# Kernel tuning notes

Measured on AMD Instinct MI355X. Metric: run time of the kernel, lower is better.

The kernel has to match this reference:

```python
import jax, jax.numpy as jnp
import numpy as np

N = 50000      # nodes
E = 800000     # edges
D = 200        # in_dim = hid_dim
R = 230        # num_rels
B = 100        # bdd bases -> submat = D // B = 2
S = D // B     # submatrix size (2)


def setup_inputs() -> dict:
    key = jax.random.key(0)
    ks = jax.random.split(key, 16)
    node_feat = jax.random.normal(ks[0], (N, D), dtype=jnp.float32)
    dynamic_emb = jax.random.normal(ks[1], (N, 1, D), dtype=jnp.float32)
    src = jax.random.randint(ks[2], (E,), 0, N, dtype=jnp.int32)
    dst = jax.random.randint(ks[3], (E,), 0, N, dtype=jnp.int32)
    etypes = jax.random.randint(ks[4], (E,), 0, R, dtype=jnp.int32)
    # BDD relational weights per layer: [R, B, S, S]
    w1 = jax.random.normal(ks[5], (R, B, S, S), dtype=jnp.float32) * 0.1
    loop_w1 = jax.random.normal(ks[6], (D, D), dtype=jnp.float32) * 0.05
    b1 = jnp.zeros((D,), dtype=jnp.float32)
    w2 = jax.random.normal(ks[7], (R, B, S, S), dtype=jnp.float32) * 0.1
    loop_w2 = jax.random.normal(ks[8], (D, D), dtype=jnp.float32) * 0.05
    b2 = jnp.zeros((D,), dtype=jnp.float32)
    # single-layer vanilla RNN (tanh) params
    W_ih = jax.random.normal(ks[9], (D, D), dtype=jnp.float32) * 0.05
    W_hh = jax.random.normal(ks[10], (D, D), dtype=jnp.float32) * 0.05
    b_ih = jnp.zeros((D,), dtype=jnp.float32)
    b_hh = jnp.zeros((D,), dtype=jnp.float32)
    return {"node_feat": node_feat, "dynamic_emb": dynamic_emb,
            "src": src, "dst": dst, "etypes": etypes,
            "w1": w1, "loop_w1": loop_w1, "b1": b1,
            "w2": w2, "loop_w2": loop_w2, "b2": b2,
            "W_ih": W_ih, "W_hh": W_hh, "b_ih": b_ih, "b_hh": b_hh}


def _rel_graph_conv_bdd(x, src, dst, etypes, edge_norm, w, loop_w, b):
    # gather source feats and apply per-edge-type block-diagonal transform
    xs = x[src].reshape(E, B, S)                     # [E, B, S]
    msg = jnp.einsum('ebi,ebio->ebo', xs, w[etypes]) # [E, B, S]
    msg = msg.reshape(E, D) * edge_norm              # edge-norm scaling
    agg = jax.ops.segment_sum(msg, dst, num_segments=N)  # scatter-add to dst
    return agg + x @ loop_w + b                      # self-loop + bias


def reference(node_feat, dynamic_emb, src, dst, etypes,
              w1, loop_w1, b1, w2, loop_w2, b2,
              W_ih, W_hh, b_ih, b_hh):
    # edge_norm = dst node norm = 1 / in-degree
    deg = jax.ops.segment_sum(jnp.ones((E,), jnp.float32), dst, num_segments=N)
    node_norm = jnp.where(deg > 0, 1.0 / jnp.maximum(deg, 1.0), 0.0)
    edge_norm = node_norm[dst][:, None]              # [E, 1]

    # RGCN layer 1 (tanh activation), layer 2 (no activation); dropout=eval
    h = _rel_graph_conv_bdd(node_feat, src, dst, etypes, edge_norm, w1, loop_w1, b1)
    h = jnp.tanh(h)
    h = _rel_graph_conv_bdd(h, src, dst, etypes, edge_norm, w2, loop_w2, b2)

    # single-step vanilla RNN: hn = tanh(x W_ih^T + b_ih + h0 W_hh^T + b_hh)
    h0 = dynamic_emb[:, 0, :]                        # [N, D]
    hn = jnp.tanh(h @ W_ih.T + b_ih + h0 @ W_hh.T + b_hh)
    return hn[:, None, :]                            # [N, 1, D]
```

## Files before the change

### kernel.cpp

```cpp
#include <hip/hip_runtime.h>

#define N_NODES 50000
#define N_EDGES 800000
#define DIM     200
#define NBLK    100
#define NRELS   230
#define NB_SCAN 196
#define KPAD    224
#define KPN     256
#define NROWPAD 50048
#define NFRAG8  (8 * 14 * 64)

typedef __attribute__((ext_vector_type(8)))  short short8;
typedef __attribute__((ext_vector_type(16))) float f32x16;

__device__ __forceinline__ unsigned short f2bf(float f) {
    unsigned u = __float_as_uint(f);
    u += 0x7fffu + ((u >> 16) & 1u);
    return (unsigned short)(u >> 16);
}

__device__ __forceinline__ float bflo(unsigned u) { return __uint_as_float(u << 16); }
__device__ __forceinline__ float bfhi(unsigned u) { return __uint_as_float(u & 0xffff0000u); }
__device__ __forceinline__ float b2f(unsigned short u) { return __uint_as_float((unsigned)u << 16); }

__device__ __forceinline__ float tanh_fast(float x) {
    float xa = fminf(fmaxf(x, -15.0f), 15.0f);
    float e = __expf(2.0f * xa);
    return (e - 1.0f) / (e + 1.0f);
}

__device__ __forceinline__ int uread(int v, int l) {
    return __builtin_amdgcn_readlane(v, l);
}

#if __has_builtin(__builtin_amdgcn_fdot2_f32_bf16)
typedef __bf16 bf16x2 __attribute__((ext_vector_type(2)));
__device__ __forceinline__ float dot2bf(unsigned a, unsigned b, float c) {
    return __builtin_amdgcn_fdot2_f32_bf16(
        __builtin_bit_cast(bf16x2, a), __builtin_bit_cast(bf16x2, b), c, false);
}
#define CMP(XU, WU, M0, M1, M2, M3)                                     \
    { M0 = dot2bf(XU.x, WU.x, M0); M1 = dot2bf(XU.x, WU.y, M1);         \
      M2 = dot2bf(XU.y, WU.z, M2); M3 = dot2bf(XU.y, WU.w, M3); }
#else
#define CMP(XU, WU, M0, M1, M2, M3)                                     \
    { float x0 = bflo(XU.x), x1 = bfhi(XU.x);                           \
      float x2 = bflo(XU.y), x3 = bfhi(XU.y);                           \
      M0 += x0 * bflo(WU.x) + x1 * bfhi(WU.x);                          \
      M1 += x0 * bflo(WU.y) + x1 * bfhi(WU.y);                          \
      M2 += x2 * bflo(WU.z) + x3 * bfhi(WU.z);                          \
      M3 += x2 * bflo(WU.w) + x3 * bfhi(WU.w); }
#endif

#define SWZ5(rr, off) ((unsigned)((rr) * 512 + (off)) ^ ((unsigned)((rr) & 15) << 4))

__global__ void deg_int_kernel(const int* __restrict__ dst, int* __restrict__ degi) {
    int e = blockIdx.x * blockDim.x + threadIdx.x;
    if (e < N_EDGES) atomicAdd(&degi[dst[e]], 1);
}

__global__ __launch_bounds__(256) void scanA(const int* __restrict__ degi,
                                             int* __restrict__ pos,
                                             int* __restrict__ bsum) {
    __shared__ int tmp[256];
    int t = threadIdx.x;
    int g = blockIdx.x * 256 + t;
    int v = (g < N_NODES) ? degi[g] : 0;
    tmp[t] = v;
    __syncthreads();
    for (int off = 1; off < 256; off <<= 1) {
        int xv = (t >= off) ? tmp[t - off] : 0;
        __syncthreads();
        tmp[t] += xv;
        __syncthreads();
    }
    if (g < N_NODES) pos[g] = tmp[t] - v;
    if (t == 255) bsum[blockIdx.x] = tmp[255];
}

__global__ __launch_bounds__(256) void scanB(int* __restrict__ bsum) {
    __shared__ int tmp[256];
    int t = threadIdx.x;
    int v = (t < NB_SCAN) ? bsum[t] : 0;
    tmp[t] = v;
    __syncthreads();
    for (int off = 1; off < 256; off <<= 1) {
        int xv = (t >= off) ? tmp[t - off] : 0;
        __syncthreads();
        tmp[t] += xv;
        __syncthreads();
    }
    if (t < NB_SCAN) bsum[t] = tmp[t] - v;
}

__global__ __launch_bounds__(256) void scanC(int* __restrict__ pos, const int* __restrict__ bsum) {
    int g = blockIdx.x * 256 + threadIdx.x;
    if (g < N_NODES) pos[g] += bsum[blockIdx.x];
}

__global__ void fill_kernel(const int* __restrict__ src, const int* __restrict__ dst,
                            const int* __restrict__ et,
                            int* __restrict__ pos, int* __restrict__ se) {
    int e = blockIdx.x * blockDim.x + threadIdx.x;
    if (e < N_EDGES) {
        int d = dst[e];
        int slot = atomicAdd(&pos[d], 1);
        se[slot] = src[e] | (et[e] << 16);
    }
}

__global__ void prep_xb(const float* __restrict__ x, unsigned short* __restrict__ o) {
    int idx = blockIdx.x * blockDim.x + threadIdx.x;
    if (idx >= NROWPAD * (KPAD / 2)) return;
    int row = idx / (KPAD / 2), cu = idx % (KPAD / 2);
    unsigned pk = 0;
    if (row < N_NODES && cu < 100) {
        float2 v = *(const float2*)(x + (size_t)row * DIM + cu * 2);
        pk = (unsigned)f2bf(v.x) | ((unsigned)f2bf(v.y) << 16);
    }
    *(unsigned*)(o + (size_t)idx * 2) = pk;
}

__global__ void prep_wb(const float* __restrict__ w, unsigned short* __restrict__ o) {
    int idx = blockIdx.x * blockDim.x + threadIdx.x;
    if (idx >= NRELS * NBLK) return;
    float4 v = *(const float4*)(w + (size_t)idx * 4);
    unsigned c0 = (unsigned)f2bf(v.x) | ((unsigned)f2bf(v.z) << 16);
    unsigned c1 = (unsigned)f2bf(v.y) | ((unsigned)f2bf(v.w) << 16);
    *(uint2*)(o + (size_t)idx * 4) = make_uint2(c0, c1);
}

__global__ void prep_fragT(const float* __restrict__ w, unsigned short* __restrict__ o) {
    int idx = blockIdx.x * blockDim.x + threadIdx.x;
    if (idx >= NFRAG8) return;
    int l = idx & 63;
    int ks = (idx >> 6) % 14;
    int nt = idx / (14 * 64);
    int n  = nt * 32 + (l & 31);
    int k0 = ks * 16 + (l >> 5) * 8;
    unsigned short v[8];
    #pragma unroll
    for (int j = 0; j < 8; ++j) {
        int k = k0 + j;
        v[j] = f2bf((n < DIM && k < DIM) ? w[k * DIM + n] : 0.0f);
    }
    *(uint4*)(o + (size_t)idx * 8) = *(uint4*)v;
}
__global__ void prep_frag(const float* __restrict__ w, unsigned short* __restrict__ o) {
    int idx = blockIdx.x * blockDim.x + threadIdx.x;
    if (idx >= NFRAG8) return;
    int l = idx & 63;
    int ks = (idx >> 6) % 14;
    int nt = idx / (14 * 64);
    int n  = nt * 32 + (l & 31);
    int k0 = ks * 16 + (l >> 5) * 8;
    unsigned short v[8];
    #pragma unroll
    for (int j = 0; j < 8; ++j) {
        int k = k0 + j;
        v[j] = f2bf((n < DIM && k < DIM) ? w[n * DIM + k] : 0.0f);
    }
    *(uint4*)(o + (size_t)idx * 8) = *(uint4*)v;
}

#define GL(QQ, XU, WU)                                                  \
    { int p_ = uread(sv, (QQ)); int s_ = p_ & 0xffff; int r_ = p_ >> 16;\
      XU = *(const uint2*)(x  + (size_t)s_ * KPAD + xoff);              \
      WU = *(const uint4*)(wb + (size_t)r_ * (NBLK * 4) + woff); }

__global__ __launch_bounds__(256) void gatherB(
        const unsigned short* __restrict__ x,
        const int*   __restrict__ se,
        const int*   __restrict__ endpos,
        const int*   __restrict__ degi,
        const unsigned short* __restrict__ wb,
        unsigned short* __restrict__ agg) {
    int node = (blockIdx.x * blockDim.x + threadIdx.x) >> 6;
    int lane = threadIdx.x & 63;
    if (node >= N_NODES) return;
    int deg = __builtin_amdgcn_readfirstlane(degi[node]);
    const bool act = (lane < 50);
    int cl   = act ? lane : 49;
    int xoff = 4 * cl;
    int woff = 8 * cl;

    if (deg == 0) {
        if (act) *(uint2*)(agg + (size_t)node * DIM + 4 * lane) = make_uint2(0u, 0u);
        return;
    }
    int end   = __builtin_amdgcn_readfirstlane(endpos[node]);
    int start = end - deg;

    float m0A = 0.f, m1A = 0.f, m2A = 0.f, m3A = 0.f;
    float m0B = 0.f, m1B = 0.f, m2B = 0.f, m3B = 0.f;

    for (int base = start; base < end; base += 64) {
        int cnt = end - base; if (cnt > 64) cnt = 64;
        int sv = se[base + (lane < cnt ? lane : cnt - 1)];

        uint2 X0 = {0,0}, X1 = {0,0}, X2 = {0,0}, X3 = {0,0};
        uint4 W0 = {0,0,0,0}, W1 = {0,0,0,0}, W2 = {0,0,0,0}, W3 = {0,0,0,0};

        GL(0, X0, W0);
        if (cnt > 1) GL(1, X1, W1);
        if (cnt > 2) GL(2, X2, W2);

        for (int q = 0; q < cnt; q += 4) {
            if (q + 3 < cnt) GL(q + 3, X3, W3);
            CMP(X0, W0, m0A, m1A, m2A, m3A);
            if (q + 4 < cnt) GL(q + 4, X0, W0);
            if (q + 1 < cnt) CMP(X1, W1, m0B, m1B, m2B, m3B);
            if (q + 5 < cnt) GL(q + 5, X1, W1);
            if (q + 2 < cnt) CMP(X2, W2, m0A, m1A, m2A, m3A);
            if (q + 6 < cnt) GL(q + 6, X2, W2);
            if (q + 3 < cnt) CMP(X3, W3, m0B, m1B, m2B, m3B);
        }
    }
    float nrm = 1.0f / (float)deg;
    if (act) {
        unsigned plo = (unsigned)f2bf((m0A + m0B) * nrm) | ((unsigned)f2bf((m1A + m1B) * nrm) << 16);
        unsigned phi = (unsigned)f2bf((m2A + m2B) * nrm) | ((unsigned)f2bf((m3A + m3B) * nrm) << 16);
        *(uint2*)(agg + (size_t)node * DIM + 4 * lane) = make_uint2(plo, phi);
    }
}

__global__ __launch_bounds__(256) void gemm1_kernel(
        unsigned short* xb_hb,
        const unsigned short* __restrict__ agg1,
        const float* __restrict__ b1,
        const unsigned short* __restrict__ w1f) {
    __shared__ __align__(16) unsigned short s_a[32 * KPN];
    int row0 = blockIdx.x * 32;
    int tid = threadIdx.x;
    for (int i = tid; i < 32 * 32; i += 256) {
        int rr = i >> 5, ch = i & 31;
        uint4 v = {0, 0, 0, 0};
        if (ch < 28) v = *(const uint4*)(xb_hb + (size_t)(row0 + rr) * KPAD + ch * 8);
        *(uint4*)((char*)s_a + SWZ5(rr, ch * 16)) = v;
    }
    __syncthreads();

    int l = tid & 63, wv = tid >> 6;
    int rl = l & 31, hl = l >> 5;
    int ntlo = wv * 2;
    const unsigned short* wb = w1f + (size_t)(ntlo * 14) * 512 + l * 8;

    f32x16 acc0 = {}, acc1 = {};
    short8 aC  = *(const short8*)((const char*)s_a + SWZ5(rl, (hl * 8) * 2));
    short8 b0C = *(const short8*)(wb);
    short8 b1C = *(const short8*)(wb + 14 * 512);
    #pragma unroll
    for (int ks = 0; ks < 13; ++ks) {
        short8 aN = {}, b0N = {}, b1N = {};
        if (ks < 12) {
            aN  = *(const short8*)((const char*)s_a + SWZ5(rl, ((ks + 1) * 16 + hl * 8) * 2));
            b0N = *(const short8*)(wb + (ks + 1) * 512);
            b1N = *(const short8*)(wb + 14 * 512 + (ks + 1) * 512);
        }
        acc0 = __builtin_amdgcn_mfma_f32_32x32x16_bf16(aC, b0C, acc0, 0, 0, 0);
        acc1 = __builtin_amdgcn_mfma_f32_32x32x16_bf16(aC, b1C, acc1, 0, 0, 0);
        aC = aN; b0C = b0N; b1C = b1N;
    }
    __syncthreads();

    #pragma unroll
    for (int t = 0; t < 2; ++t) {
        f32x16 ac = t ? acc1 : acc0;
        int gc = (ntlo + t) * 32 + rl;
        if (gc >= KPAD) continue;
        float bias = (gc < DIM) ? b1[gc] : 0.0f;
        #pragma unroll
        for (int r = 0; r < 16; ++r) {
            int gr = row0 + (r & 3) + 8 * (r >> 2) + 4 * hl;
            float v = 0.0f;
            if (gc < DIM && gr < N_NODES)
                v = ac[r] + b2f(agg1[(size_t)gr * DIM + gc]) + bias;
            xb_hb[(size_t)gr * KPAD + gc] = f2bf(tanh_fast(v));
        }
    }
}

__global__ __launch_bounds__(256) void gemm2_kernel(
        const unsigned short* __restrict__ hb,
        const unsigned short* __restrict__ agg2,
        const float* __restrict__ b2,
        const unsigned short* __restrict__ w2f,
        const unsigned short* __restrict__ h0b,
        const unsigned short* __restrict__ wihf,
        const unsigned short* __restrict__ whhf,
        const float* __restrict__ b_ih,
        const float* __restrict__ b_hh,
        float* __restrict__ out) {
    __shared__ __align__(16) unsigned short s_a[32 * KPN];
    __shared__ __align__(16) unsigned short t_lds[32 * KPN];
    int row0 = blockIdx.x * 32;
    int tid = threadIdx.x;
    int l = tid & 63, wv = tid >> 6;
    int rl = l & 31, hl = l >> 5;
    int ntlo = wv * 2;

    for (int i = tid; i < 32 * 32; i += 256) {
        int rr = i >> 5, ch = i & 31;
        uint4 v = {0, 0, 0, 0};
        if (ch < 28) v = *(const uint4*)(hb + (size_t)(row0 + rr) * KPAD + ch * 8);
        *(uint4*)((char*)s_a + SWZ5(rr, ch * 16)) = v;
    }
    __syncthreads();

    {
        const unsigned short* wb = w2f + (size_t)(ntlo * 14) * 512 + l * 8;
        f32x16 acc0 = {}, acc1 = {};
        short8 aC  = *(const short8*)((const char*)s_a + SWZ5(rl, (hl * 8) * 2));
        short8 b0C = *(const short8*)(wb);
        short8 b1C = *(const short8*)(wb + 14 * 512);
        #pragma unroll
        for (int ks = 0; ks < 13; ++ks) {
            short8 aN = {}, b0N = {}, b1N = {};
            if (ks < 12) {
                aN  = *(const short8*)((const char*)s_a + SWZ5(rl, ((ks + 1) * 16 + hl * 8) * 2));
                b0N = *(const short8*)(wb + (ks + 1) * 512);
                b1N = *(const short8*)(wb + 14 * 512 + (ks + 1) * 512);
            }
            acc0 = __builtin_amdgcn_mfma_f32_32x32x16_bf16(aC, b0C, acc0, 0, 0, 0);
            acc1 = __builtin_amdgcn_mfma_f32_32x32x16_bf16(aC, b1C, acc1, 0, 0, 0);
            aC = aN; b0C = b0N; b1C = b1N;
        }
        #pragma unroll
        for (int t = 0; t < 2; ++t) {
            f32x16 ac = t ? acc1 : acc0;
            int gc = (ntlo + t) * 32 + rl;
            float bias = (gc < DIM) ? b2[gc] : 0.0f;
            #pragma unroll
            for (int r = 0; r < 16; ++r) {
                int lr = (r & 3) + 8 * (r >> 2) + 4 * hl;
                int gr = row0 + lr;
                float v = 0.0f;
                if (gc < DIM) {
                    v = ac[r] + bias;
                    if (gr < N_NODES) v += b2f(agg2[(size_t)gr * DIM + gc]);
                }
                *(unsigned short*)((char*)t_lds + SWZ5(lr, gc * 2)) = f2bf(v);
            }
        }
    }
    __syncthreads();

    for (int i = tid; i < 32 * 32; i += 256) {
        int rr = i >> 5, ch = i & 31;
        uint4 v = {0, 0, 0, 0};
        if (ch < 28) v = *(const uint4*)(h0b + (size_t)(row0 + rr) * KPAD + ch * 8);
        *(uint4*)((char*)s_a + SWZ5(rr, ch * 16)) = v;
    }
    __syncthreads();

    {
        const unsigned short* wi = wihf + (size_t)(ntlo * 14) * 512 + l * 8;
        const unsigned short* wh = whhf + (size_t)(ntlo * 14) * 512 + l * 8;
        f32x16 o0 = {}, o1 = {};
        short8 tC  = *(const short8*)((const char*)t_lds + SWZ5(rl, (hl * 8) * 2));
        short8 fC  = *(const short8*)((const char*)s_a  + SWZ5(rl, (hl * 8) * 2));
        short8 i0C = *(const short8*)(wi);
        short8 i1C = *(const short8*)(wi + 14 * 512);
        short8 h0C = *(const short8*)(wh);
        short8 h1C = *(const short8*)(wh + 14 * 512);
        #pragma unroll
        for (int ks = 0; ks < 13; ++ks) {
            short8 tN = {}, fN = {}, i0N = {}, i1N = {}, h0N = {}, h1N = {};
            if (ks < 12) {
                unsigned off = ((ks + 1) * 16 + hl * 8) * 2;
                tN  = *(const short8*)((const char*)t_lds + SWZ5(rl, off));
                fN  = *(const short8*)((const char*)s_a  + SWZ5(rl, off));
                i0N = *(const short8*)(wi + (ks + 1) * 512);
                i1N = *(const short8*)(wi + 14 * 512 + (ks + 1) * 512);
                h0N = *(const short8*)(wh + (ks + 1) * 512);
                h1N = *(const short8*)(wh + 14 * 512 + (ks + 1) * 512);
            }
            o0 = __builtin_amdgcn_mfma_f32_32x32x16_bf16(tC, i0C, o0, 0, 0, 0);
            o0 = __builtin_amdgcn_mfma_f32_32x32x16_bf16(fC, h0C, o0, 0, 0, 0);
            o1 = __builtin_amdgcn_mfma_f32_32x32x16_bf16(tC, i1C, o1, 0, 0, 0);
            o1 = __builtin_amdgcn_mfma_f32_32x32x16_bf16(fC, h1C, o1, 0, 0, 0);
            tC = tN; fC = fN; i0C = i0N; i1C = i1N; h0C = h0N; h1C = h1N;
        }
        #pragma unroll
        for (int t = 0; t < 2; ++t) {
            f32x16 oc = t ? o1 : o0;
            int gc = (ntlo + t) * 32 + rl;
            if (gc >= DIM) continue;
            float bias = b_ih[gc] + b_hh[gc];
            #pragma unroll
            for (int r = 0; r < 16; ++r) {
                int gr = row0 + (r & 3) + 8 * (r >> 2) + 4 * hl;
                if (gr < N_NODES)
                    out[(size_t)gr * DIM + gc] = tanh_fast(oc[r] + bias);
            }
        }
    }
}

extern "C" void kernel_launch(void* const* d_in, const int* in_sizes, int n_in,
                              void* d_out, int out_size, void* d_ws, size_t ws_size,
                              hipStream_t stream) {
    const float* node_feat = (const float*)d_in[0];
    const float* dyn_emb   = (const float*)d_in[1];
    const int*   src       = (const int*)  d_in[2];
    const int*   dst       = (const int*)  d_in[3];
    const int*   etypes    = (const int*)  d_in[4];
    const float* w1        = (const float*)d_in[5];
    const float* loop_w1   = (const float*)d_in[6];
    const float* b1        = (const float*)d_in[7];
    const float* w2        = (const float*)d_in[8];
    const float* loop_w2   = (const float*)d_in[9];
    const float* b2        = (const float*)d_in[10];
    const float* W_ih      = (const float*)d_in[11];
    const float* W_hh      = (const float*)d_in[12];
    const float* b_ih      = (const float*)d_in[13];
    const float* b_hh      = (const float*)d_in[14];
    float* out = (float*)d_out;

    int*   degi = (int*)d_ws;
    int*   pos  = degi + 51200;
    int*   bsum = pos  + 51200;
    int*   se   = bsum + 256;
    unsigned short* agg = (unsigned short*)(se + N_EDGES);
    unsigned short* hb   = agg  + (size_t)N_NODES * DIM;
    unsigned short* h0b  = hb   + (size_t)NROWPAD * KPAD;
    unsigned short* w1f  = h0b  + (size_t)NROWPAD * KPAD;
    unsigned short* w2f  = w1f  + (size_t)NFRAG8 * 8;
    unsigned short* wihf = w2f  + (size_t)NFRAG8 * 8;
    unsigned short* whhf = wihf + (size_t)NFRAG8 * 8;
    unsigned short* w1b  = whhf + (size_t)NFRAG8 * 8;
    unsigned short* w2b  = w1b  + (size_t)NRELS * NBLK * 4;

    hipMemsetAsync(degi, 0, 51200 * sizeof(int), stream);

    deg_int_kernel<<<(N_EDGES + 255) / 256, 256, 0, stream>>>(dst, degi);
    scanA<<<NB_SCAN, 256, 0, stream>>>(degi, pos, bsum);
    scanB<<<1, 256, 0, stream>>>(bsum);
    scanC<<<NB_SCAN, 256, 0, stream>>>(pos, bsum);
    fill_kernel<<<(N_EDGES + 255) / 256, 256, 0, stream>>>(src, dst, etypes, pos, se);

    prep_xb<<<(NROWPAD * (KPAD / 2) + 255) / 256, 256, 0, stream>>>(node_feat, hb);
    prep_xb<<<(NROWPAD * (KPAD / 2) + 255) / 256, 256, 0, stream>>>(dyn_emb, h0b);
    prep_wb<<<(NRELS * NBLK + 255) / 256, 256, 0, stream>>>(w1, w1b);
    prep_wb<<<(NRELS * NBLK + 255) / 256, 256, 0, stream>>>(w2, w2b);
    prep_fragT<<<(NFRAG8 + 255) / 256, 256, 0, stream>>>(loop_w1, w1f);
    prep_fragT<<<(NFRAG8 + 255) / 256, 256, 0, stream>>>(loop_w2, w2f);
    prep_frag <<<(NFRAG8 + 255) / 256, 256, 0, stream>>>(W_ih, wihf);
    prep_frag <<<(NFRAG8 + 255) / 256, 256, 0, stream>>>(W_hh, whhf);

    gatherB<<<(N_NODES * 64 + 255) / 256, 256, 0, stream>>>(
        hb, se, pos, degi, w1b, agg);
    gemm1_kernel<<<(N_NODES + 31) / 32, 256, 0, stream>>>(
        hb, agg, b1, w1f);

    gatherB<<<(N_NODES * 64 + 255) / 256, 256, 0, stream>>>(
        hb, se, pos, degi, w2b, agg);

    gemm2_kernel<<<(N_NODES + 31) / 32, 256, 0, stream>>>(
        hb, agg, b2, w2f, h0b, wihf, whhf, b_ih, b_hh, out);
}
```

Before: 348.2 us.

## Fold layer-2 self-loop weight into RNN input weight and merge prep kernels

Precomputes M = loop_w2 · W_ih^T and a combined bias so the final kernel computes h·M + agg·W_ih^T + h0·W_hh^T in one MFMA pass. This removes the intermediate bf16 tile in LDS, one sync phase and a separate GEMM stage. The agg buffer becomes KPAD-padded so it can be staged like the other operands. Several small prep and scan launches are also merged into fewer kernels. In exchange, the final kernel issues three MFMAs per k-step instead of two sequential GEMMs, and the folded weights are rounded differently (M is rounded to bf16 once rather than the intermediate result).

Measured after the change: 367.8 us. 1.06x slower.

```diff
diff --git a/kernel.cpp b/kernel.cpp
--- a/kernel.cpp
+++ b/kernel.cpp
@@ -79,8 +79,9 @@
     if (t == 255) bsum[blockIdx.x] = tmp[255];
 }
 
-__global__ __launch_bounds__(256) void scanB(int* __restrict__ bsum) {
+__global__ __launch_bounds__(256) void scanC2(int* __restrict__ pos, const int* __restrict__ bsum) {
     __shared__ int tmp[256];
+    __shared__ int excl[256];
     int t = threadIdx.x;
     int v = (t < NB_SCAN) ? bsum[t] : 0;
     tmp[t] = v;
@@ -91,12 +92,11 @@
         tmp[t] += xv;
         __syncthreads();
     }
-    if (t < NB_SCAN) bsum[t] = tmp[t] - v;
-}
-
-__global__ __launch_bounds__(256) void scanC(int* __restrict__ pos, const int* __restrict__ bsum) {
-    int g = blockIdx.x * 256 + threadIdx.x;
-    if (g < N_NODES) pos[g] += bsum[blockIdx.x];
+    excl[t] = tmp[t] - v;
+    __syncthreads();
+    int add = excl[blockIdx.x];
+    int g = blockIdx.x * 256 + t;
+    if (g < N_NODES) pos[g] += add;
 }
 
 __global__ void fill_kernel(const int* __restrict__ src, const int* __restrict__ dst,
@@ -110,58 +110,97 @@
     }
 }
 
-__global__ void prep_xb(const float* __restrict__ x, unsigned short* __restrict__ o) {
+__global__ void prep_feat(const float* __restrict__ x, const float* __restrict__ de,
+                          unsigned short* __restrict__ hb, unsigned short* __restrict__ h0b) {
+    const int HALF = NROWPAD * (KPAD / 2);
     int idx = blockIdx.x * blockDim.x + threadIdx.x;
-    if (idx >= NROWPAD * (KPAD / 2)) return;
-    int row = idx / (KPAD / 2), cu = idx % (KPAD / 2);
+    if (idx >= 2 * HALF) return;
+    const float* src = (idx < HALF) ? x : de;
+    unsigned short* dstp = (idx < HALF) ? hb : h0b;
+    int j = (idx < HALF) ? idx : idx - HALF;
+    int row = j / (KPAD / 2), cu = j % (KPAD / 2);
     unsigned pk = 0;
     if (row < N_NODES && cu < 100) {
-        float2 v = *(const float2*)(x + (size_t)row * DIM + cu * 2);
+        float2 v = *(const float2*)(src + (size_t)row * DIM + cu * 2);
         pk = (unsigned)f2bf(v.x) | ((unsigned)f2bf(v.y) << 16);
     }
-    *(unsigned*)(o + (size_t)idx * 2) = pk;
-}
-
-__global__ void prep_wb(const float* __restrict__ w, unsigned short* __restrict__ o) {
+    *(unsigned*)(dstp + (size_t)j * 2) = pk;
+}
+
+__global__ void prep_wbs(const float* __restrict__ w1, const float* __restrict__ w2,
+                         unsigned short* __restrict__ w1b, unsigned short* __restrict__ w2b) {
+    const int HALF = NRELS * NBLK;
     int idx = blockIdx.x * blockDim.x + threadIdx.x;
-    if (idx >= NRELS * NBLK) return;
-    float4 v = *(const float4*)(w + (size_t)idx * 4);
+    if (idx >= 2 * HALF) return;
+    const float* w = (idx < HALF) ? w1 : w2;
+    unsigned short* o = (idx < HALF) ? w1b : w2b;
+    int j = (idx < HALF) ? idx : idx - HALF;
+    float4 v = *(const float4*)(w + (size_t)j * 4);
     unsigned c0 = (unsigned)f2bf(v.x) | ((unsigned)f2bf(v.z) << 16);
     unsigned c1 = (unsigned)f2bf(v.y) | ((unsigned)f2bf(v.w) << 16);
-    *(uint2*)(o + (size_t)idx * 4) = make_uint2(c0, c1);
-}
-
-__global__ void prep_fragT(const float* __restrict__ w, unsigned short* __restrict__ o) {
+    *(uint2*)(o + (size_t)j * 4) = make_uint2(c0, c1);
+}
+
+__global__ void prep_frags(const float* __restrict__ lw1, const float* __restrict__ wih,
+                           const float* __restrict__ whh,
+                           unsigned short* __restrict__ w1f, unsigned short* __restrict__ wihf,
+                           unsigned short* __restrict__ whhf) {
     int idx = blockIdx.x * blockDim.x + threadIdx.x;
-    if (idx >= NFRAG8) return;
-    int l = idx & 63;
-    int ks = (idx >> 6) % 14;
-    int nt = idx / (14 * 64);
+    if (idx >= 3 * NFRAG8) return;
+    int sec = idx / NFRAG8, f = idx % NFRAG8;
+    const float* w = (sec == 0) ? lw1 : (sec == 1) ? wih : whh;
+    unsigned short* o = (sec == 0) ? w1f : (sec == 1) ? wihf : whhf;
+    int l = f & 63;
+    int ks = (f >> 6) % 14;
+    int nt = f / (14 * 64);
     int n  = nt * 32 + (l & 31);
     int k0 = ks * 16 + (l >> 5) * 8;
     unsigned short v[8];
     #pragma unroll
     for (int j = 0; j < 8; ++j) {
         int k = k0 + j;
-        v[j] = f2bf((n < DIM && k < DIM) ? w[k * DIM + n] : 0.0f);
-    }
-    *(uint4*)(o + (size_t)idx * 8) = *(uint4*)v;
-}
-__global__ void prep_frag(const float* __restrict__ w, unsigned short* __restrict__ o) {
+        float val = 0.0f;
+        if (n < DIM && k < DIM)
+            val = (sec == 0) ? w[k * DIM + n] : w[n * DIM + k];
+        v[j] = f2bf(val);
+    }
+    *(uint4*)(o + (size_t)f * 8) = *(uint4*)v;
+}
+
+__global__ void prep_Mf(const float* __restrict__ w2, const float* __restrict__ wih,
+                        const float* __restrict__ b2, const float* __restrict__ b_ih,
+                        const float* __restrict__ b_hh,
+                        unsigned short* __restrict__ Mf, float* __restrict__ biasv) {
     int idx = blockIdx.x * blockDim.x + threadIdx.x;
-    if (idx >= NFRAG8) return;
-    int l = idx & 63;
-    int ks = (idx >> 6) % 14;
-    int nt = idx / (14 * 64);
-    int n  = nt * 32 + (l & 31);
-    int k0 = ks * 16 + (l >> 5) * 8;
-    unsigned short v[8];
-    #pragma unroll
-    for (int j = 0; j < 8; ++j) {
-        int k = k0 + j;
-        v[j] = f2bf((n < DIM && k < DIM) ? w[n * DIM + k] : 0.0f);
-    }
-    *(uint4*)(o + (size_t)idx * 8) = *(uint4*)v;
+    if (idx < NFRAG8) {
+        int l = idx & 63;
+        int ks = (idx >> 6) % 14;
+        int nt = idx / (14 * 64);
+        int n  = nt * 32 + (l & 31);
+        int k0 = ks * 16 + (l >> 5) * 8;
+        unsigned short v[8];
+        #pragma unroll
+        for (int j = 0; j < 8; ++j) {
+            int k = k0 + j;
+            float s = 0.0f;
+            if (n < DIM && k < DIM) {
+                const float* wr = w2 + (size_t)k * DIM;
+                const float* ir = wih + (size_t)n * DIM;
+                for (int q = 0; q < DIM; ++q) s += wr[q] * ir[q];
+            }
+            v[j] = f2bf(s);
+        }
+        *(uint4*)(Mf + (size_t)idx * 8) = *(uint4*)v;
+    } else if (idx < NFRAG8 + KPN) {
+        int n = idx - NFRAG8;
+        float s = 0.0f;
+        if (n < DIM) {
+            const float* ir = wih + (size_t)n * DIM;
+            for (int q = 0; q < DIM; ++q) s += b2[q] * ir[q];
+            s += b_ih[n] + b_hh[n];
+        }
+        biasv[n] = s;
+    }
 }
 
 #define GL(QQ, XU, WU)                                                  \
@@ -186,7 +225,7 @@
     int woff = 8 * cl;
 
     if (deg == 0) {
-        if (act) *(uint2*)(agg + (size_t)node * DIM + 4 * lane) = make_uint2(0u, 0u);
+        if (lane < 56) *(uint2*)(agg + (size_t)node * KPAD + 4 * lane) = make_uint2(0u, 0u);
         return;
     }
     int end   = __builtin_amdgcn_readfirstlane(endpos[node]);
@@ -218,11 +257,12 @@
         }
     }
     float nrm = 1.0f / (float)deg;
+    uint2 ov = make_uint2(0u, 0u);
     if (act) {
-        unsigned plo = (unsigned)f2bf((m0A + m0B) * nrm) | ((unsigned)f2bf((m1A + m1B) * nrm) << 16);
-        unsigned phi = (unsigned)f2bf((m2A + m2B) * nrm) | ((unsigned)f2bf((m3A + m3B) * nrm) << 16);
-        *(uint2*)(agg + (size_t)node * DIM + 4 * lane) = make_uint2(plo, phi);
-    }
+        ov.x = (unsigned)f2bf((m0A + m0B) * nrm) | ((unsigned)f2bf((m1A + m1B) * nrm) << 16);
+        ov.y = (unsigned)f2bf((m2A + m2B) * nrm) | ((unsigned)f2bf((m3A + m3B) * nrm) << 16);
+    }
+    if (lane < 56) *(uint2*)(agg + (size_t)node * KPAD + 4 * lane) = ov;
 }
 
 __global__ __launch_bounds__(256) void gemm1_kernel(
@@ -275,7 +315,7 @@
             int gr = row0 + (r & 3) + 8 * (r >> 2) + 4 * hl;
             float v = 0.0f;
             if (gc < DIM && gr < N_NODES)
-                v = ac[r] + b2f(agg1[(size_t)gr * DIM + gc]) + bias;
+                v = ac[r] + b2f(agg1[(size_t)gr * KPAD + gc]) + bias;
             xb_hb[(size_t)gr * KPAD + gc] = f2bf(tanh_fast(v));
         }
     }
@@ -283,117 +323,89 @@
 
 __global__ __launch_bounds__(256) void gemm2_kernel(
         const unsigned short* __restrict__ hb,
-        const unsigned short* __restrict__ agg2,
-        const float* __restrict__ b2,
-        const unsigned short* __restrict__ w2f,
+        const unsigned short* __restrict__ aggp,
         const unsigned short* __restrict__ h0b,
+        const unsigned short* __restrict__ Mf,
         const unsigned short* __restrict__ wihf,
         const unsigned short* __restrict__ whhf,
-        const float* __restrict__ b_ih,
-        const float* __restrict__ b_hh,
+        const float* __restrict__ biasv,
         float* __restrict__ out) {
-    __shared__ __align__(16) unsigned short s_a[32 * KPN];
-    __shared__ __align__(16) unsigned short t_lds[32 * KPN];
+    __shared__ __align__(16) unsigned short s_h[32 * KPN];
+    __shared__ __align__(16) unsigned short s_g[32 * KPN];
+    __shared__ __align__(16) unsigned short s_e[32 * KPN];
     int row0 = blockIdx.x * 32;
     int tid = threadIdx.x;
+    for (int i = tid; i < 32 * 32; i += 256) {
+        int rr = i >> 5, ch = i & 31;
+        uint4 vh = {0,0,0,0}, vg = {0,0,0,0}, ve = {0,0,0,0};
+        if (ch < 28) {
+            size_t off = (size_t)(row0 + rr) * KPAD + ch * 8;
+            vh = *(const uint4*)(hb   + off);
+            vg = *(const uint4*)(aggp + off);
+            ve = *(const uint4*)(h0b  + off);
+        }
+        unsigned sw = SWZ5(rr, ch * 16);
+        *(uint4*)((char*)s_h + sw) = vh;
+        *(uint4*)((char*)s_g + sw) = vg;
+        *(uint4*)((char*)s_e + sw) = ve;
+    }
+    __syncthreads();
+
     int l = tid & 63, wv = tid >> 6;
     int rl = l & 31, hl = l >> 5;
     int ntlo = wv * 2;
-
-    for (int i = tid; i < 32 * 32; i += 256) {
-        int rr = i >> 5, ch = i & 31;
-        uint4 v = {0, 0, 0, 0};
-        if (ch < 28) v = *(const uint4*)(hb + (size_t)(row0 + rr) * KPAD + ch * 8);
-        *(uint4*)((char*)s_a + SWZ5(rr, ch * 16)) = v;
-    }
-    __syncthreads();
-
-    {
-        const unsigned short* wb = w2f + (size_t)(ntlo * 14) * 512 + l * 8;
-        f32x16 acc0 = {}, acc1 = {};
-        short8 aC  = *(const short8*)((const char*)s_a + SWZ5(rl, (hl * 8) * 2));
-        short8 b0C = *(const short8*)(wb);
-        short8 b1C = *(const short8*)(wb + 14 * 512);
+    const unsigned short* pm = Mf   + (size_t)(ntlo * 14) * 512 + l * 8;
+    const unsigned short* pi = wihf + (size_t)(ntlo * 14) * 512 + l * 8;
+    const unsigned short* ph = whhf + (size_t)(ntlo * 14) * 512 + l * 8;
+
+    f32x16 a0 = {}, a1 = {};
+    unsigned off0 = SWZ5(rl, (hl * 8) * 2);
+    short8 hC  = *(const short8*)((const char*)s_h + off0);
+    short8 gC  = *(const short8*)((const char*)s_g + off0);
+    short8 eC  = *(const short8*)((const char*)s_e + off0);
+    short8 m0C = *(const short8*)(pm);
+    short8 m1C = *(const short8*)(pm + 14 * 512);
+    short8 i0C = *(const short8*)(pi);
+    short8 i1C = *(const short8*)(pi + 14 * 512);
+    short8 h0C = *(const short8*)(ph);
+    short8 h1C = *(const short8*)(ph + 14 * 512);
+    #pragma unroll
+    for (int ks = 0; ks < 13; ++ks) {
+        short8 hN = {}, gN = {}, eN = {};
+        short8 m0N = {}, m1N = {}, i0N = {}, i1N = {}, h0N = {}, h1N = {};
+        if (ks < 12) {
+            unsigned off = SWZ5(rl, ((ks + 1) * 16 + hl * 8) * 2);
+            hN  = *(const short8*)((const char*)s_h + off);
+            gN  = *(const short8*)((const char*)s_g + off);
+            eN  = *(const short8*)((const char*)s_e + off);
+            m0N = *(const short8*)(pm + (ks + 1) * 512);
+            m1N = *(const short8*)(pm + 14 * 512 + (ks + 1) * 512);
+            i0N = *(const short8*)(pi + (ks + 1) * 512);
+            i1N = *(const short8*)(pi + 14 * 512 + (ks + 1) * 512);
+            h0N = *(const short8*)(ph + (ks + 1) * 512);
+            h1N = *(const short8*)(ph + 14 * 512 + (ks + 1) * 512);
+        }
+        a0 = __builtin_amdgcn_mfma_f32_32x32x16_bf16(hC, m0C, a0, 0, 0, 0);
+        a0 = __builtin_amdgcn_mfma_f32_32x32x16_bf16(gC, i0C, a0, 0, 0, 0);
+        a0 = __builtin_amdgcn_mfma_f32_32x32x16_bf16(eC, h0C, a0, 0, 0, 0);
+        a1 = __builtin_amdgcn_mfma_f32_32x32x16_bf16(hC, m1C, a1, 0, 0, 0);
+        a1 = __builtin_amdgcn_mfma_f32_32x32x16_bf16(gC, i1C, a1, 0, 0, 0);
+        a1 = __builtin_amdgcn_mfma_f32_32x32x16_bf16(eC, h1C, a1, 0, 0, 0);
+        hC = hN; gC = gN; eC = eN;
+        m0C = m0N; m1C = m1N; i0C = i0N; i1C = i1N; h0C = h0N; h1C = h1N;
+    }
+
+    #pragma unroll
+    for (int t = 0; t < 2; ++t) {
+        f32x16 oc = t ? a1 : a0;
+        int gc = (ntlo + t) * 32 + rl;
+        if (gc >= DIM) continue;
+        float bias = biasv[gc];
         #pragma unroll
-        for (int ks = 0; ks < 13; ++ks) {
-            short8 aN = {}, b0N = {}, b1N = {};
-            if (ks < 12) {
-                aN  = *(const short8*)((const char*)s_a + SWZ5(rl, ((ks + 1) * 16 + hl * 8) * 2));
-                b0N = *(const short8*)(wb + (ks + 1) * 512);
-                b1N = *(const short8*)(wb + 14 * 512 + (ks + 1) * 512);
-            }
-            acc0 = __builtin_amdgcn_mfma_f32_32x32x16_bf16(aC, b0C, acc0, 0, 0, 0);
-            acc1 = __builtin_amdgcn_mfma_f32_32x32x16_bf16(aC, b1C, acc1, 0, 0, 0);
-            aC = aN; b0C = b0N; b1C = b1N;
-        }
-        #pragma unroll
-        for (int t = 0; t < 2; ++t) {
-            f32x16 ac = t ? acc1 : acc0;
-            int gc = (ntlo + t) * 32 + rl;
-            float bias = (gc < DIM) ? b2[gc] : 0.0f;
-            #pragma unroll
-            for (int r = 0; r < 16; ++r) {
-                int lr = (r & 3) + 8 * (r >> 2) + 4 * hl;
-                int gr = row0 + lr;
-                float v = 0.0f;
-                if (gc < DIM) {
-                    v = ac[r] + bias;
-                    if (gr < N_NODES) v += b2f(agg2[(size_t)gr * DIM + gc]);
-                }
-                *(unsigned short*)((char*)t_lds + SWZ5(lr, gc * 2)) = f2bf(v);
-            }
-        }
-    }
-    __syncthreads();
-
-    for (int i = tid; i < 32 * 32; i += 256) {
-        int rr = i >> 5, ch = i & 31;
-        uint4 v = {0, 0, 0, 0};
-        if (ch < 28) v = *(const uint4*)(h0b + (size_t)(row0 + rr) * KPAD + ch * 8);
-        *(uint4*)((char*)s_a + SWZ5(rr, ch * 16)) = v;
-    }
-    __syncthreads();
-
-    {
-        const unsigned short* wi = wihf + (size_t)(ntlo * 14) * 512 + l * 8;
-        const unsigned short* wh = whhf + (size_t)(ntlo * 14) * 512 + l * 8;
-        f32x16 o0 = {}, o1 = {};
-        short8 tC  = *(const short8*)((const char*)t_lds + SWZ5(rl, (hl * 8) * 2));
-        short8 fC  = *(const short8*)((const char*)s_a  + SWZ5(rl, (hl * 8) * 2));
-        short8 i0C = *(const short8*)(wi);
-        short8 i1C = *(const short8*)(wi + 14 * 512);
-        short8 h0C = *(const short8*)(wh);
-        short8 h1C = *(const short8*)(wh + 14 * 512);
-        #pragma unroll
-        for (int ks = 0; ks < 13; ++ks) {
-            short8 tN = {}, fN = {}, i0N = {}, i1N = {}, h0N = {}, h1N = {};
-            if (ks < 12) {
-                unsigned off = ((ks + 1) * 16 + hl * 8) * 2;
-                tN  = *(const short8*)((const char*)t_lds + SWZ5(rl, off));
-                fN  = *(const short8*)((const char*)s_a  + SWZ5(rl, off));
-                i0N = *(const short8*)(wi + (ks + 1) * 512);
-                i1N = *(const short8*)(wi + 14 * 512 + (ks + 1) * 512);
-                h0N = *(const short8*)(wh + (ks + 1) * 512);
-                h1N = *(const short8*)(wh + 14 * 512 + (ks + 1) * 512);
-            }
-            o0 = __builtin_amdgcn_mfma_f32_32x32x16_bf16(tC, i0C, o0, 0, 0, 0);
-            o0 = __builtin_amdgcn_mfma_f32_32x32x16_bf16(fC, h0C, o0, 0, 0, 0);
-            o1 = __builtin_amdgcn_mfma_f32_32x32x16_bf16(tC, i1C, o1, 0, 0, 0);
-            o1 = __builtin_amdgcn_mfma_f32_32x32x16_bf16(fC, h1C, o1, 0, 0, 0);
-            tC = tN; fC = fN; i0C = i0N; i1C = i1N; h0C = h0N; h1C = h1N;
-        }
-        #pragma unroll
-        for (int t = 0; t < 2; ++t) {
-            f32x16 oc = t ? o1 : o0;
-            int gc = (ntlo + t) * 32 + rl;
-            if (gc >= DIM) continue;
-            float bias = b_ih[gc] + b_hh[gc];
-            #pragma unroll
-            for (int r = 0; r < 16; ++r) {
-                int gr = row0 + (r & 3) + 8 * (r >> 2) + 4 * hl;
-                if (gr < N_NODES)
-                    out[(size_t)gr * DIM + gc] = tanh_fast(oc[r] + bias);
-            }
+        for (int r = 0; r < 16; ++r) {
+            int gr = row0 + (r & 3) + 8 * (r >> 2) + 4 * hl;
+            if (gr < N_NODES)
+                out[(size_t)gr * DIM + gc] = tanh_fast(oc[r] + bias);
         }
     }
 }
@@ -422,41 +434,40 @@
     int*   pos  = degi + 51200;
     int*   bsum = pos  + 51200;
     int*   se   = bsum + 256;
-    unsigned short* agg = (unsigned short*)(se + N_EDGES);
-    unsigned short* hb   = agg  + (size_t)N_NODES * DIM;
+    unsigned short* aggp = (unsigned short*)(se + N_EDGES);
+    unsigned short* hb   = aggp + (size_t)NROWPAD * KPAD;
     unsigned short* h0b  = hb   + (size_t)NROWPAD * KPAD;
     unsigned short* w1f  = h0b  + (size_t)NROWPAD * KPAD;
-    unsigned short* w2f  = w1f  + (size_t)NFRAG8 * 8;
-    unsigned short* wihf = w2f  + (size_t)NFRAG8 * 8;
+    unsigned short* wihf = w1f  + (size_t)NFRAG8 * 8;
     unsigned short* whhf = wihf + (size_t)NFRAG8 * 8;
-    unsigned short* w1b  = whhf + (size_t)NFRAG8 * 8;
+    unsigned short* Mf   = whhf + (size_t)NFRAG8 * 8;
+    unsigned short* w1b  = Mf   + (size_t)NFRAG8 * 8;
     unsigned short* w2b  = w1b  + (size_t)NRELS * NBLK * 4;
+    float* biasv = (float*)(w2b + (size_t)NRELS * NBLK * 4);
 
     hipMemsetAsync(degi, 0, 51200 * sizeof(int), stream);
 
     deg_int_kernel<<<(N_EDGES + 255) / 256, 256, 0, stream>>>(dst, degi);
     scanA<<<NB_SCAN, 256, 0, stream>>>(degi, pos, bsum);
-    scanB<<<1, 256, 0, stream>>>(bsum);
-    scanC<<<NB_SCAN, 256, 0, stream>>>(pos, bsum);
+    scanC2<<<NB_SCAN, 256, 0, stream>>>(pos, bsum);
     fill_kernel<<<(N_EDGES + 255) / 256, 256, 0, stream>>>(src, dst, etypes, pos, se);
 
-    prep_xb<<<(NROWPAD * (KPAD / 2) + 255) / 256, 256, 0, stream>>>(node_feat, hb);
-    prep_xb<<<(NROWPAD * (KPAD / 2) + 255) / 256, 256, 0, stream>>>(dyn_emb, h0b);
-    prep_wb<<<(NRELS * NBLK + 255) / 256, 256, 0, stream>>>(w1, w1b);
-    prep_wb<<<(NRELS * NBLK + 255) / 256, 256, 0, stream>>>(w2, w2b);
-    prep_fragT<<<(NFRAG8 + 255) / 256, 256, 0, stream>>>(loop_w1, w1f);
-    prep_fragT<<<(NFRAG8 + 255) / 256, 256, 0, stream>>>(loop_w2, w2f);
-    prep_frag <<<(NFRAG8 + 255) / 256, 256, 0, stream>>>(W_ih, wihf);
-    prep_frag <<<(NFRAG8 + 255) / 256, 256, 0, stream>>>(W_hh, whhf);
+    prep_feat<<<(2 * NROWPAD * (KPAD / 2) + 255) / 256, 256, 0, stream>>>(
+        node_feat, dyn_emb, hb, h0b);
+    prep_wbs<<<(2 * NRELS * NBLK + 255) / 256, 256, 0, stream>>>(w1, w2, w1b, w2b);
+    prep_frags<<<(3 * NFRAG8 + 255) / 256, 256, 0, stream>>>(
+        loop_w1, W_ih, W_hh, w1f, wihf, whhf);
+    prep_Mf<<<(NFRAG8 + KPN + 255) / 256, 256, 0, stream>>>(
+        loop_w2, W_ih, b2, b_ih, b_hh, Mf, biasv);
 
     gatherB<<<(N_NODES * 64 + 255) / 256, 256, 0, stream>>>(
-        hb, se, pos, degi, w1b, agg);
+        hb, se, pos, degi, w1b, aggp);
     gemm1_kernel<<<(N_NODES + 31) / 32, 256, 0, stream>>>(
-        hb, agg, b1, w1f);
+        hb, aggp, b1, w1f);
 
     gatherB<<<(N_NODES * 64 + 255) / 256, 256, 0, stream>>>(
-        hb, se, pos, degi, w2b, agg);
+        hb, se, pos, degi, w2b, aggp);
 
     gemm2_kernel<<<(N_NODES + 31) / 32, 256, 0, stream>>>(
-        hb, agg, b2, w2f, h0b, wihf, whhf, b_ih, b_hh, out);
-}
+        hb, aggp, h0b, Mf, wihf, whhf, biasv, out);
+}
```
